# Performance work log

Hardware: AMD Instinct MI355X
Metric: run time of the kernel (lower is better)

The kernel has to match this reference:

```python
import jax, jax.numpy as jnp
import numpy as np

S, B, F, H, L, T = 256, 64, 256, 768, 3, 32  # seq_len, batch, features, hidden, layers, target_len


def setup_inputs() -> dict:
    key = jax.random.key(0)
    ks = jax.random.split(key, 16)
    s = 1.0 / np.sqrt(H)  # PyTorch LSTM/Linear uniform init bound
    u = lambda k, shape: jax.random.uniform(k, shape, jnp.float32, -s, s)
    return {
        "x": jax.random.normal(ks[0], (S, B, F), jnp.float32),
        # encoder layer 0: input_size -> hidden_size
        "e_Wih0": u(ks[1], (4 * H, F)), "e_Whh0": u(ks[2], (4 * H, H)),
        "e_bih0": u(ks[3], (4 * H,)), "e_bhh0": u(ks[4], (4 * H,)),
        # encoder layers 1..L-1 (stacked): hidden -> hidden
        "e_Wih": u(ks[5], (L - 1, 4 * H, H)), "e_Whh": u(ks[6], (L - 1, 4 * H, H)),
        "e_bih": u(ks[7], (L - 1, 4 * H)), "e_bhh": u(ks[8], (L - 1, 4 * H)),
        # decoder layers (stacked): hidden -> hidden
        "d_Wih": u(ks[9], (L, 4 * H, H)), "d_Whh": u(ks[10], (L, 4 * H, H)),
        "d_bih": u(ks[11], (L, 4 * H)), "d_bhh": u(ks[12], (L, 4 * H)),
        # output head: hidden -> input_size
        "lin_W": u(ks[13], (F, H)), "lin_b": u(ks[14], (F,)),
        "target_len": T,
    }


def _cell(gates, c_prev):
    # PyTorch gate order: input, forget, cell(g), output
    i, f, g, o = jnp.split(gates, 4, axis=-1)
    c = jax.nn.sigmoid(f) * c_prev + jax.nn.sigmoid(i) * jnp.tanh(g)
    h = jax.nn.sigmoid(o) * jnp.tanh(c)
    return h, c


def reference(x, e_Wih0, e_Whh0, e_bih0, e_bhh0, e_Wih, e_Whh, e_bih, e_bhh,
              d_Wih, d_Whh, d_bih, d_bhh, lin_W, lin_b, target_len):
    Bb = x.shape[1]
    Hh = e_Whh0.shape[1]
    dt = x.dtype

    # --- encoder layer 0: full-sequence LSTM from zero state ---
    b0 = e_bih0 + e_bhh0
    def enc_step(carry, x_t):
        h, c = carry
        h, c = _cell(x_t @ e_Wih0.T + h @ e_Whh0.T + b0, c)
        return (h, c), None
    z = jnp.zeros((Bb, Hh), dt)
    (h, _), _ = jax.lax.scan(enc_step, (z, z), x)

    # --- encoder layers 1..L-1: each sees previous layer's final hidden as a
    # seq_len=1 input with fresh zero (h0, c0) -> W_hh term vanishes ---
    enc = [h]
    xin = h
    for l in range(e_Wih.shape[0]):
        hl, _ = _cell(xin @ e_Wih[l].T + (e_bih[l] + e_bhh[l]), 0.0)
        enc.append(hl)
        xin = hl
    encoder_hidden = jnp.stack(enc)  # (L, B, H)

    # --- decoder: recursive. Call-site bug passes zeros as initial hidden_list.
    # Each step, each layer i independently runs a 1-step LSTM on its own previous
    # hidden with fresh zero state (W_hh unused, cell not carried). Only the last
    # layer's hidden feeds the Linear head. ---
    d_b = (d_bih + d_bhh)[:, None, :]  # (L, 1, 4H)
    def dec_step(hs, _):
        gates = jnp.einsum('lbh,lgh->lbg', hs, d_Wih) + d_b
        hn, _ = _cell(gates, 0.0)
        out_t = hn[-1] @ lin_W.T + lin_b  # (B, F)
        return hn, out_t
    h0 = jnp.zeros((d_Wih.shape[0], Bb, Hh), dt)
    _, outputs = jax.lax.scan(dec_step, h0, None, length=target_len)  # (T, B, F)

    return outputs, encoder_hidden
```

## Files before the change

### kernel.cpp

```cpp
#include <hip/hip_runtime.h>
#include <hip/hip_bf16.h>


constexpr int NB = 64;
constexpr int NH = 768;
constexpr int NF = 256;
constexpr int NS = 256;
constexpr int NT = 32;
constexpr int ENC_BLOCKS = 96;
constexpr int ENC_GROUP  = 48;
constexpr int DEC_BLOCKS = 48;

typedef short bf16x8 __attribute__((ext_vector_type(8)));
typedef float f32x4 __attribute__((ext_vector_type(4)));

__device__ __forceinline__ float sigm(float x) { return 1.f / (1.f + expf(-x)); }

__device__ __forceinline__ int4 ld_i4_cohere(const int4* p) {
    int4 v;
    asm volatile("global_load_dwordx4 %0, %1, off sc0 sc1" : "=v"(v) : "v"(p));
    return v;
}
__device__ __forceinline__ int ld_i1_cohere_sync(const int* p) {
    int v;
    asm volatile("global_load_dword %0, %1, off sc0 sc1\n\ts_waitcnt vmcnt(0)"
                 : "=v"(v) : "v"(p) : "memory");
    return v;
}
__device__ __forceinline__ void st_i1_cohere(int* p, int v) {
    asm volatile("global_store_dword %0, %1, off sc0 sc1" :: "v"(p), "v"(v) : "memory");
}
__device__ __forceinline__ void vm_drain() {
    asm volatile("s_waitcnt vmcnt(0)" ::: "memory");
}

__device__ __forceinline__ void arrive(int* slots, int idx, int phase) {
    if (threadIdx.x == 0) st_i1_cohere(slots + idx * 16, phase);
}
__device__ __forceinline__ void wait_all(int* slots, int phase, int nb) {
    if (threadIdx.x < nb) {
        const int* p = slots + threadIdx.x * 16;
        while (ld_i1_cohere_sync(p) < phase) __builtin_amdgcn_s_sleep(1);
    }
    __syncthreads();
}

__global__ __launch_bounds__(256) void cvt_all(
    const float* __restrict__ s0,
    const float* __restrict__ s1,
    const float* __restrict__ s2,
    const float* __restrict__ s3,
    __hip_bfloat16* __restrict__ d)
{
    const int i = (blockIdx.x * 256 + threadIdx.x) * 4;
    const float* s; int off;
    if (i < 4194304)      { s = s0; off = 0; }
    else if (i < 4980736) { s = s1; off = 4194304; }
    else if (i < 7340032) { s = s2; off = 4980736; }
    else                  { s = s3; off = 7340032; }
    const float4 v = *(const float4*)(s + (i - off));
    d[i]     = __float2bfloat16(v.x);
    d[i + 1] = __float2bfloat16(v.y);
    d[i + 2] = __float2bfloat16(v.z);
    d[i + 3] = __float2bfloat16(v.w);
}

__global__ __launch_bounds__(256, 1) void enc_dec_persist(
    const __hip_bfloat16* __restrict__ xb,
    const __hip_bfloat16* __restrict__ Wx,
    const __hip_bfloat16* __restrict__ Wh,
    const float* __restrict__ bih, const float* __restrict__ bhh,
    int* __restrict__ h0buf,
    int* __restrict__ h1buf,
    float* __restrict__ enc0,
    int* slots,
    const float* __restrict__ dW,
    const float* __restrict__ dbih, const float* __restrict__ dbhh,
    float* __restrict__ hd0, float* __restrict__ hd1,
    float* __restrict__ hall, int* dslots)
{
    __shared__ int   hst[32 * 388];
    __shared__ float gbuf[4][32][17];
    __shared__ float lbias[64];
    __shared__ float hstD[768];

    const int tid = threadIdx.x;

    if (blockIdx.x >= ENC_BLOCKS) {
        const int dbid = blockIdx.x - ENC_BLOCKS;
        const int ul = tid >> 4;
        const int j  = tid & 15;
        const int u  = dbid * 16 + ul;
        const float* Wi = dW + (size_t)u * NH;
        const float* Wg = dW + (size_t)(2 * NH + u) * NH;
        const float* Wo = dW + (size_t)(3 * NH + u) * NH;
        const float bi = dbih[u]          + dbhh[u];
        const float bg = dbih[2 * NH + u] + dbhh[2 * NH + u];
        const float bo = dbih[3 * NH + u] + dbhh[3 * NH + u];

        for (int t = 0; t < NT; ++t) {
            const float* hin = (t & 1) ? hd1 : hd0;
            float* hout      = (t & 1) ? hd0 : hd1;
            if (t > 0) wait_all(dslots, t, DEC_BLOCKS);
            if (tid < 192) {
                int4 v = ld_i4_cohere((const int4*)hin + tid);
                vm_drain();
                ((int4*)hstD)[tid] = v;
            }
            __syncthreads();
            float ai = 0.f, ag = 0.f, ao = 0.f;
            for (int k = j; k < NH; k += 16) {
                const float hv = hstD[k];
                ai += hv * Wi[k];
                ag += hv * Wg[k];
                ao += hv * Wo[k];
            }
            #pragma unroll
            for (int off = 8; off > 0; off >>= 1) {
                ai += __shfl_xor(ai, off, 16);
                ag += __shfl_xor(ag, off, 16);
                ao += __shfl_xor(ao, off, 16);
            }
            if (j == 0) {
                const float cn = sigm(ai + bi) * tanhf(ag + bg);
                const float hn = sigm(ao + bo) * tanhf(cn);
                hall[(size_t)t * NH + u] = hn;
                if (t < NT - 1)
                    st_i1_cohere((int*)(hout + u), __float_as_int(hn));
            }
            if (t < NT - 1) {
                vm_drain();
                __syncthreads();
                arrive(dslots, dbid, t + 1);
            }
        }
        return;
    }

    const int bu = blockIdx.x % (NH / 16);
    const int bm = blockIdx.x / (NH / 16);
    int* gslots = slots + bm * ENC_GROUP * 16;
    const int u0 = bu * 16;
    const int g = tid >> 6;
    const int lane = tid & 63;
    const int r = lane & 15;
    const int q = lane >> 4;
    const int row0 = bm * 32 + r;
    const int row1 = row0 + 16;

    const size_t wrow = (size_t)(g * NH + u0 + r);
    bf16x8 wx[8], wh[24];
    #pragma unroll
    for (int c = 0; c < 8; ++c)
        wx[c] = *(const bf16x8*)(Wx + wrow * NF + c * 32 + q * 8);
    #pragma unroll
    for (int c = 0; c < 24; ++c)
        wh[c] = *(const bf16x8*)(Wh + wrow * NH + c * 32 + q * 8);

    if (tid < 64)
        lbias[tid] = bih[(tid >> 4) * NH + u0 + (tid & 15)]
                   + bhh[(tid >> 4) * NH + u0 + (tid & 15)];
    __syncthreads();

    float cst[2] = {0.f, 0.f};

    for (int t = 0; t < NS; ++t) {
        const int* hcur = (t & 1) ? h1buf : h0buf;
        int* hnext      = (t & 1) ? h0buf : h1buf;
        const __hip_bfloat16* xt = xb + (size_t)t * NB * NF;

        f32x4 acc0 = {0.f, 0.f, 0.f, 0.f};
        f32x4 acc1 = {0.f, 0.f, 0.f, 0.f};
        #pragma unroll
        for (int c = 0; c < 8; ++c) {
            const bf16x8 a0 = *(const bf16x8*)(xt + (size_t)row0 * NF + c * 32 + q * 8);
            const bf16x8 a1 = *(const bf16x8*)(xt + (size_t)row1 * NF + c * 32 + q * 8);
            acc0 = __builtin_amdgcn_mfma_f32_16x16x32_bf16(a0, wx[c], acc0, 0, 0, 0);
            acc1 = __builtin_amdgcn_mfma_f32_16x16x32_bf16(a1, wx[c], acc1, 0, 0, 0);
        }

        if (t > 0) wait_all(gslots, t, ENC_GROUP);

        {
            const int4* src = (const int4*)hcur + bm * 3072;
            int4 v[12];
            #pragma unroll
            for (int i = 0; i < 12; ++i) v[i] = ld_i4_cohere(src + i * 256 + tid);
            vm_drain();
            #pragma unroll
            for (int i = 0; i < 12; ++i) {
                const int k = i * 256 + tid;
                const int rw = k / 96, cl = k % 96;
                *(int4*)(hst + rw * 388 + cl * 4) = v[i];
            }
        }
        __syncthreads();

        #pragma unroll
        for (int c = 0; c < 24; ++c) {
            const bf16x8 a0 = *(const bf16x8*)((const short*)hst + r * 776 + c * 32 + q * 8);
            const bf16x8 a1 = *(const bf16x8*)((const short*)hst + (r + 16) * 776 + c * 32 + q * 8);
            acc0 = __builtin_amdgcn_mfma_f32_16x16x32_bf16(a0, wh[c], acc0, 0, 0, 0);
            acc1 = __builtin_amdgcn_mfma_f32_16x16x32_bf16(a1, wh[c], acc1, 0, 0, 0);
        }

        #pragma unroll
        for (int i = 0; i < 4; ++i) {
            gbuf[g][q * 4 + i][r]      = acc0[i];
            gbuf[g][16 + q * 4 + i][r] = acc1[i];
        }
        __syncthreads();

        {
            const int rowl = tid >> 3, pair = tid & 7;
            const int ua = pair * 2;
            float h2[2];
            #pragma unroll
            for (int e = 0; e < 2; ++e) {
                const int ul = ua + e;
                const float pi = gbuf[0][rowl][ul] + lbias[ul];
                const float pf = gbuf[1][rowl][ul] + lbias[16 + ul];
                const float pg = gbuf[2][rowl][ul] + lbias[32 + ul];
                const float po = gbuf[3][rowl][ul] + lbias[48 + ul];
                const float cn = sigm(pf) * cst[e] + sigm(pi) * tanhf(pg);
                h2[e] = sigm(po) * tanhf(cn);
                cst[e] = cn;
            }
            const int b = bm * 32 + rowl;
            if (t == NS - 1) {
                enc0[(size_t)b * NH + u0 + ua]     = h2[0];
                enc0[(size_t)b * NH + u0 + ua + 1] = h2[1];
                __hip_bfloat16* hf = (__hip_bfloat16*)hnext;
                hf[(size_t)b * NH + u0 + ua]     = __float2bfloat16(h2[0]);
                hf[(size_t)b * NH + u0 + ua + 1] = __float2bfloat16(h2[1]);
            } else {
                union { __hip_bfloat16 b16; unsigned short s; } c0, c1;
                c0.b16 = __float2bfloat16(h2[0]);
                c1.b16 = __float2bfloat16(h2[1]);
                const int pv = (int)c0.s | ((int)c1.s << 16);
                st_i1_cohere(hnext + (size_t)b * 384 + (u0 >> 1) + pair, pv);
            }
        }
        if (t < NS - 1) {
            vm_drain();
            __syncthreads();
            arrive(gslots, bu, t + 1);
        }
    }
}

template<int KX, int KH>
__global__ __launch_bounds__(256) void lstm_step(
    const __hip_bfloat16* __restrict__ xin,
    const __hip_bfloat16* __restrict__ hin,
    const __hip_bfloat16* __restrict__ Wx,
    const __hip_bfloat16* __restrict__ Wh,
    const float* __restrict__ bih, const float* __restrict__ bhh,
    const float* __restrict__ c_in,
    __hip_bfloat16* __restrict__ h_bf,
    float* __restrict__ h_f32,
    float* __restrict__ c_out)
{
    constexpr int K = KX + KH;
    constexpr int NCH = K / 32;
    const int bu = blockIdx.x % (NH / 16);
    const int bm = blockIdx.x / (NH / 16);
    const int u0 = bu * 16;
    const int tid = threadIdx.x;
    const int g = tid >> 6;
    const int lane = tid & 63;
    const int r = lane & 15;
    const int q = lane >> 4;

    f32x4 acc0 = {0.f, 0.f, 0.f, 0.f};
    f32x4 acc1 = {0.f, 0.f, 0.f, 0.f};
    const int row0 = bm * 32 + r;
    const int row1 = row0 + 16;
    const long wr = (long)(g * NH + u0 + r);

    #pragma unroll
    for (int c = 0; c < NCH; ++c) {
        const int k0 = c * 32;
        bf16x8 a0, a1, bfrag;
        if (k0 < KX) {
            const int kk = k0 + q * 8;
            a0 = *(const bf16x8*)(xin + (long)row0 * KX + kk);
            a1 = *(const bf16x8*)(xin + (long)row1 * KX + kk);
            bfrag = *(const bf16x8*)(Wx + wr * KX + kk);
        } else {
            const int kk = (k0 - KX) + q * 8;
            a0 = *(const bf16x8*)(hin + (long)row0 * KH + kk);
            a1 = *(const bf16x8*)(hin + (long)row1 * KH + kk);
            bfrag = *(const bf16x8*)(Wh + wr * KH + kk);
        }
        acc0 = __builtin_amdgcn_mfma_f32_16x16x32_bf16(a0, bfrag, acc0, 0, 0, 0);
        acc1 = __builtin_amdgcn_mfma_f32_16x16x32_bf16(a1, bfrag, acc1, 0, 0, 0);
    }

    __shared__ float gbuf[4][32][17];
    #pragma unroll
    for (int i = 0; i < 4; ++i) {
        gbuf[g][q * 4 + i][r]      = acc0[i];
        gbuf[g][16 + q * 4 + i][r] = acc1[i];
    }
    __syncthreads();

    #pragma unroll
    for (int i = 0; i < 2; ++i) {
        const int idx = tid + i * 256;
        const int bl = idx >> 4;
        const int u  = idx & 15;
        const int gu = u0 + u;
        const int b  = bm * 32 + bl;
        const float pi = gbuf[0][bl][u] + bih[gu]          + bhh[gu];
        const float pf = gbuf[1][bl][u] + bih[NH + gu]     + bhh[NH + gu];
        const float pg = gbuf[2][bl][u] + bih[2 * NH + gu] + bhh[2 * NH + gu];
        const float po = gbuf[3][bl][u] + bih[3 * NH + gu] + bhh[3 * NH + gu];
        const float cp = c_in ? c_in[(long)b * NH + gu] : 0.f;
        const float cn = sigm(pf) * cp + sigm(pi) * tanhf(pg);
        const float hn = sigm(po) * tanhf(cn);
        if (c_out) c_out[(long)b * NH + gu] = cn;
        if (h_f32) h_f32[(long)b * NH + gu] = hn;
        h_bf[(long)b * NH + gu] = __float2bfloat16(hn);
    }
}

__global__ __launch_bounds__(256) void head_kernel(
    const float* __restrict__ hall,
    const float* __restrict__ lw,
    const float* __restrict__ lb,
    float* __restrict__ out)
{
    const int t = blockIdx.x;
    const int f = threadIdx.x;
    const float* h = hall + (size_t)t * NH;
    const float4* wrow = (const float4*)(lw + (size_t)f * NH);
    float acc = 0.f;
    for (int k4 = 0; k4 < NH / 4; ++k4) {
        const float4 w = wrow[k4];
        acc += h[k4 * 4]     * w.x;
        acc += h[k4 * 4 + 1] * w.y;
        acc += h[k4 * 4 + 2] * w.z;
        acc += h[k4 * 4 + 3] * w.w;
    }
    acc += lb[f];
    float* o = out + (size_t)t * NB * NF + f;
    for (int b = 0; b < NB; ++b) o[(size_t)b * NF] = acc;
}

extern "C" void kernel_launch(void* const* d_in, const int* in_sizes, int n_in,
                              void* d_out, int out_size, void* d_ws, size_t ws_size,
                              hipStream_t stream) {
    (void)in_sizes; (void)n_in; (void)out_size; (void)ws_size;
    const float* x     = (const float*)d_in[0];
    const float* eWih0 = (const float*)d_in[1];
    const float* eWhh0 = (const float*)d_in[2];
    const float* ebih0 = (const float*)d_in[3];
    const float* ebhh0 = (const float*)d_in[4];
    const float* eWih  = (const float*)d_in[5];
    const float* ebih  = (const float*)d_in[7];
    const float* ebhh  = (const float*)d_in[8];
    const float* dWih  = (const float*)d_in[9];
    const float* dbih  = (const float*)d_in[11];
    const float* dbhh  = (const float*)d_in[12];
    const float* linW  = (const float*)d_in[13];
    const float* linb  = (const float*)d_in[14];
    float* out = (float*)d_out;

    char* ws = (char*)d_ws;
    __hip_bfloat16* xb   = (__hip_bfloat16*)(ws);
    __hip_bfloat16* W0x  = (__hip_bfloat16*)(ws +  8388608);
    __hip_bfloat16* W0h  = (__hip_bfloat16*)(ws +  9961472);
    __hip_bfloat16* eW12 = (__hip_bfloat16*)(ws + 14680064);
    int* hbi0 = (int*)(ws + 24117248);
    int* hbi1 = (int*)(ws + 24215552);
    float* hd0  = (float*)(ws + 24313856);
    float* hd1  = (float*)(ws + 24316928);
    float* hall = (float*)(ws + 24320000);
    int* bar    = (int*)(ws + 24418304);
    int* enc_slots = bar;
    int* dec_slots = bar + 2048;

    (void)hipMemsetAsync(hbi0, 0, (size_t)NB * NH * 2, stream);
    (void)hipMemsetAsync(hd0, 0, (size_t)NH * 4, stream);
    (void)hipMemsetAsync(bar, 0, 16384, stream);

    cvt_all<<<12058624 / 1024, 256, 0, stream>>>(x, eWih0, eWhh0, eWih,
                                                 (__hip_bfloat16*)ws);

    float* enc = out + (size_t)NT * NB * NF;

    const float* W2 = dWih + (size_t)2 * 4 * NH * NH;
    enc_dec_persist<<<ENC_BLOCKS + DEC_BLOCKS, 256, 0, stream>>>(
        xb, W0x, W0h, ebih0, ebhh0, hbi0, hbi1, enc, enc_slots,
        W2, dbih + 2 * 4 * NH, dbhh + 2 * 4 * NH, hd0, hd1, hall, dec_slots);

    __hip_bfloat16* hb0 = (__hip_bfloat16*)hbi0;
    __hip_bfloat16* hb1 = (__hip_bfloat16*)hbi1;
    lstm_step<NH, 0><<<96, 256, 0, stream>>>(
        hb0, nullptr, eW12, nullptr, ebih, ebhh,
        nullptr, hb1, enc + NB * NH, nullptr);
    lstm_step<NH, 0><<<96, 256, 0, stream>>>(
        hb1, nullptr, eW12 + (size_t)4 * NH * NH, nullptr,
        ebih + 4 * NH, ebhh + 4 * NH,
        nullptr, hb0, enc + 2 * (size_t)NB * NH, nullptr);

    head_kernel<<<NT, NF, 0, stream>>>(hall, linW, linb, out);
}
```

Before: 1.561 ms.

## Replace encoder slot barrier with per-element step-tagged hidden-state exchange

Drops the per-step group barrier (arrive and wait on 48 slots) in the encoder recurrence. Each hidden-state pair is now stored together with its step number as an 8-byte tagged word in a double buffer, and readers poll the tags until every needed element carries the current step. This removes the store drain, block sync and barrier round trip on each step, so a block can proceed as soon as its data lands. The cost is doubled exchange traffic, repeated polling loads, and a bounded spin that could proceed with stale data if it times out.

```diff
diff --git a/kernel.cpp b/kernel.cpp
--- a/kernel.cpp
+++ b/kernel.cpp
@@ -8,8 +8,8 @@
 constexpr int NS = 256;
 constexpr int NT = 32;
 constexpr int ENC_BLOCKS = 96;
-constexpr int ENC_GROUP  = 48;
 constexpr int DEC_BLOCKS = 48;
+constexpr size_t HXBUF = 196608;
 
 typedef short bf16x8 __attribute__((ext_vector_type(8)));
 typedef float f32x4 __attribute__((ext_vector_type(4)));
@@ -30,8 +30,36 @@
 __device__ __forceinline__ void st_i1_cohere(int* p, int v) {
     asm volatile("global_store_dword %0, %1, off sc0 sc1" :: "v"(p), "v"(v) : "memory");
 }
+__device__ __forceinline__ void st_i2_cohere(void* p, int2 v) {
+    asm volatile("global_store_dwordx2 %0, %1, off sc0 sc1" :: "v"(p), "v"(v) : "memory");
+}
 __device__ __forceinline__ void vm_drain() {
     asm volatile("s_waitcnt vmcnt(0)" ::: "memory");
+    __builtin_amdgcn_sched_barrier(0);
+}
+
+__device__ __forceinline__ void ld8_i4_cohere_sync(
+    const int4* p0, const int4* p1, const int4* p2, const int4* p3,
+    const int4* p4, const int4* p5, const int4* p6, const int4* p7,
+    int4& w0, int4& w1, int4& w2, int4& w3,
+    int4& w4, int4& w5, int4& w6, int4& w7)
+{
+    asm volatile(
+        "global_load_dwordx4 %0, %8, off sc0 sc1\n\t"
+        "global_load_dwordx4 %1, %9, off sc0 sc1\n\t"
+        "global_load_dwordx4 %2, %10, off sc0 sc1\n\t"
+        "global_load_dwordx4 %3, %11, off sc0 sc1\n\t"
+        "global_load_dwordx4 %4, %12, off sc0 sc1\n\t"
+        "global_load_dwordx4 %5, %13, off sc0 sc1\n\t"
+        "global_load_dwordx4 %6, %14, off sc0 sc1\n\t"
+        "global_load_dwordx4 %7, %15, off sc0 sc1\n\t"
+        "s_waitcnt vmcnt(0)"
+        : "=&v"(w0), "=&v"(w1), "=&v"(w2), "=&v"(w3),
+          "=&v"(w4), "=&v"(w5), "=&v"(w6), "=&v"(w7)
+        : "v"(p0), "v"(p1), "v"(p2), "v"(p3),
+          "v"(p4), "v"(p5), "v"(p6), "v"(p7)
+        : "memory");
+    __builtin_amdgcn_sched_barrier(0);
 }
 
 __device__ __forceinline__ void arrive(int* slots, int idx, int phase) {
@@ -70,10 +98,9 @@
     const __hip_bfloat16* __restrict__ Wx,
     const __hip_bfloat16* __restrict__ Wh,
     const float* __restrict__ bih, const float* __restrict__ bhh,
-    int* __restrict__ h0buf,
-    int* __restrict__ h1buf,
+    char* __restrict__ hxt,
+    __hip_bfloat16* __restrict__ hfin,
     float* __restrict__ enc0,
-    int* slots,
     const float* __restrict__ dW,
     const float* __restrict__ dbih, const float* __restrict__ dbhh,
     float* __restrict__ hd0, float* __restrict__ hd1,
@@ -139,7 +166,6 @@
 
     const int bu = blockIdx.x % (NH / 16);
     const int bm = blockIdx.x / (NH / 16);
-    int* gslots = slots + bm * ENC_GROUP * 16;
     const int u0 = bu * 16;
     const int g = tid >> 6;
     const int lane = tid & 63;
@@ -164,9 +190,12 @@
 
     float cst[2] = {0.f, 0.f};
 
+    const int rowl = tid >> 3, pair = tid & 7;
+    const int bsto = bm * 32 + rowl;
+    char* const slot_even = hxt + HXBUF + ((size_t)bsto * 384 + bu * 8 + pair) * 8;
+    char* const slot_odd  = hxt +         ((size_t)bsto * 384 + bu * 8 + pair) * 8;
+
     for (int t = 0; t < NS; ++t) {
-        const int* hcur = (t & 1) ? h1buf : h0buf;
-        int* hnext      = (t & 1) ? h0buf : h1buf;
         const __hip_bfloat16* xt = xb + (size_t)t * NB * NF;
 
         f32x4 acc0 = {0.f, 0.f, 0.f, 0.f};
@@ -179,19 +208,34 @@
             acc1 = __builtin_amdgcn_mfma_f32_16x16x32_bf16(a1, wx[c], acc1, 0, 0, 0);
         }
 
-        if (t > 0) wait_all(gslots, t, ENC_GROUP);
-
         {
-            const int4* src = (const int4*)hcur + bm * 3072;
-            int4 v[12];
+            const int4* src = (const int4*)(hxt + (size_t)(t & 1) * HXBUF)
+                            + bm * 6144 + tid;
             #pragma unroll
-            for (int i = 0; i < 12; ++i) v[i] = ld_i4_cohere(src + i * 256 + tid);
-            vm_drain();
-            #pragma unroll
-            for (int i = 0; i < 12; ++i) {
-                const int k = i * 256 + tid;
-                const int rw = k / 96, cl = k % 96;
-                *(int4*)(hst + rw * 388 + cl * 4) = v[i];
+            for (int pass = 0; pass < 3; ++pass) {
+                const int base = pass * 8;
+                unsigned done = 0;
+                int spin = 0;
+                while (done != 0xFFu && ++spin < 8192) {
+                    int4 w0, w1, w2, w3, w4, w5, w6, w7;
+                    ld8_i4_cohere_sync(
+                        src + (base + 0) * 256, src + (base + 1) * 256,
+                        src + (base + 2) * 256, src + (base + 3) * 256,
+                        src + (base + 4) * 256, src + (base + 5) * 256,
+                        src + (base + 6) * 256, src + (base + 7) * 256,
+                        w0, w1, w2, w3, w4, w5, w6, w7);
+                    const int4 wa[8] = {w0, w1, w2, w3, w4, w5, w6, w7};
+                    #pragma unroll
+                    for (int i = 0; i < 8; ++i) {
+                        if (!(done & (1u << i)) && wa[i].y == t && wa[i].w == t) {
+                            const int f  = ((base + i) * 256 + tid) * 2;
+                            const int rw = f / 384, pc = f % 384;
+                            *(int2*)((char*)hst + rw * 1552 + pc * 4)
+                                = make_int2(wa[i].x, wa[i].z);
+                            done |= 1u << i;
+                        }
+                    }
+                }
             }
         }
         __syncthreads();
@@ -212,7 +256,6 @@
         __syncthreads();
 
         {
-            const int rowl = tid >> 3, pair = tid & 7;
             const int ua = pair * 2;
             float h2[2];
             #pragma unroll
@@ -226,25 +269,18 @@
                 h2[e] = sigm(po) * tanhf(cn);
                 cst[e] = cn;
             }
-            const int b = bm * 32 + rowl;
             if (t == NS - 1) {
-                enc0[(size_t)b * NH + u0 + ua]     = h2[0];
-                enc0[(size_t)b * NH + u0 + ua + 1] = h2[1];
-                __hip_bfloat16* hf = (__hip_bfloat16*)hnext;
-                hf[(size_t)b * NH + u0 + ua]     = __float2bfloat16(h2[0]);
-                hf[(size_t)b * NH + u0 + ua + 1] = __float2bfloat16(h2[1]);
+                enc0[(size_t)bsto * NH + u0 + ua]     = h2[0];
+                enc0[(size_t)bsto * NH + u0 + ua + 1] = h2[1];
+                hfin[(size_t)bsto * NH + u0 + ua]     = __float2bfloat16(h2[0]);
+                hfin[(size_t)bsto * NH + u0 + ua + 1] = __float2bfloat16(h2[1]);
             } else {
                 union { __hip_bfloat16 b16; unsigned short s; } c0, c1;
                 c0.b16 = __float2bfloat16(h2[0]);
                 c1.b16 = __float2bfloat16(h2[1]);
                 const int pv = (int)c0.s | ((int)c1.s << 16);
-                st_i1_cohere(hnext + (size_t)b * 384 + (u0 >> 1) + pair, pv);
-            }
-        }
-        if (t < NS - 1) {
-            vm_drain();
-            __syncthreads();
-            arrive(gslots, bu, t + 1);
+                st_i2_cohere((t & 1) ? slot_odd : slot_even, make_int2(pv, t + 1));
+            }
         }
     }
 }
@@ -372,16 +408,16 @@
     __hip_bfloat16* W0x  = (__hip_bfloat16*)(ws +  8388608);
     __hip_bfloat16* W0h  = (__hip_bfloat16*)(ws +  9961472);
     __hip_bfloat16* eW12 = (__hip_bfloat16*)(ws + 14680064);
-    int* hbi0 = (int*)(ws + 24117248);
-    int* hbi1 = (int*)(ws + 24215552);
-    float* hd0  = (float*)(ws + 24313856);
-    float* hd1  = (float*)(ws + 24316928);
-    float* hall = (float*)(ws + 24320000);
-    int* bar    = (int*)(ws + 24418304);
-    int* enc_slots = bar;
-    int* dec_slots = bar + 2048;
-
-    (void)hipMemsetAsync(hbi0, 0, (size_t)NB * NH * 2, stream);
+    char* hxt  = ws + 24117248;
+    __hip_bfloat16* hfin = (__hip_bfloat16*)(ws + 24510464);
+    __hip_bfloat16* hmid = (__hip_bfloat16*)(ws + 24608768);
+    float* hd0  = (float*)(ws + 24707072);
+    float* hd1  = (float*)(ws + 24710144);
+    float* hall = (float*)(ws + 24713216);
+    int* bar    = (int*)(ws + 24811520);
+    int* dec_slots = bar;
+
+    (void)hipMemsetAsync(hxt, 0, 2 * HXBUF, stream);
     (void)hipMemsetAsync(hd0, 0, (size_t)NH * 4, stream);
     (void)hipMemsetAsync(bar, 0, 16384, stream);
 
@@ -392,18 +428,16 @@
 
     const float* W2 = dWih + (size_t)2 * 4 * NH * NH;
     enc_dec_persist<<<ENC_BLOCKS + DEC_BLOCKS, 256, 0, stream>>>(
-        xb, W0x, W0h, ebih0, ebhh0, hbi0, hbi1, enc, enc_slots,
+        xb, W0x, W0h, ebih0, ebhh0, hxt, hfin, enc,
         W2, dbih + 2 * 4 * NH, dbhh + 2 * 4 * NH, hd0, hd1, hall, dec_slots);
 
-    __hip_bfloat16* hb0 = (__hip_bfloat16*)hbi0;
-    __hip_bfloat16* hb1 = (__hip_bfloat16*)hbi1;
     lstm_step<NH, 0><<<96, 256, 0, stream>>>(
-        hb0, nullptr, eW12, nullptr, ebih, ebhh,
-        nullptr, hb1, enc + NB * NH, nullptr);
+        hfin, nullptr, eW12, nullptr, ebih, ebhh,
+        nullptr, hmid, enc + NB * NH, nullptr);
     lstm_step<NH, 0><<<96, 256, 0, stream>>>(
-        hb1, nullptr, eW12 + (size_t)4 * NH * NH, nullptr,
+        hmid, nullptr, eW12 + (size_t)4 * NH * NH, nullptr,
         ebih + 4 * NH, ebhh + 4 * NH,
-        nullptr, hb0, enc + 2 * (size_t)NB * NH, nullptr);
+        nullptr, hfin, enc + 2 * (size_t)NB * NH, nullptr);
 
     head_kernel<<<NT, NF, 0, stream>>>(hall, linW, linb, out);
 }
```

Result: slower. 1.618 ms (+3.7%).
